# Performance work log

Measured on AMD Instinct MI355X. Metric: run time of the kernel, lower is better.

The kernel has to match this reference:

```python
import jax, jax.numpy as jnp
import numpy as np

EPS = 1e-5

def _ln(x):
    # F.layer_norm over last dim, no affine params
    m = jnp.mean(x, axis=-1, keepdims=True)
    v = jnp.mean((x - m) ** 2, axis=-1, keepdims=True)
    return (x - m) * jax.lax.rsqrt(v + EPS)

def _jagged_to_padded(vals, offsets, B, n):
    # vals: [T, F] -> [B, n, F], zero padded
    T = vals.shape[0]
    lengths = offsets[1:] - offsets[:-1]            # [B]
    pos = jnp.arange(n)
    idx = offsets[:-1, None] + pos[None, :]         # [B, n]
    valid = pos[None, :] < lengths[:, None]         # [B, n]
    gathered = vals[jnp.clip(idx, 0, T - 1)]        # [B, n, F]
    return jnp.where(valid[..., None], gathered, 0.0)

def _dense_to_jagged(padded, offsets, T):
    # padded: [B, n, F] -> [T, F]
    t = jnp.arange(T)
    b = jnp.clip(jnp.searchsorted(offsets, t, side='right') - 1, 0, offsets.shape[0] - 2)
    pos = t - offsets[b]
    return padded[b, pos]

def setup_inputs() -> dict:
    key = jax.random.key(0)
    D, H, d = 1024, 8, 128
    B, n = 4, 2048
    T = B * n  # all sequences full length
    ks = jax.random.split(key, 4)
    x = jax.random.normal(ks[0], (T, D), dtype=jnp.float32)
    attnmask = jnp.tril(jnp.ones((n, n), dtype=jnp.float32))
    x_offsets = jnp.arange(B + 1, dtype=jnp.int32) * n
    proj_w = jax.random.normal(ks[1], (D, H * d * 4), dtype=jnp.float32) * 0.02
    out_w = jax.random.normal(ks[2], (H * d, D), dtype=jnp.float32) * 0.02
    out_b = jnp.zeros((D,), dtype=jnp.float32)
    return {"x": x, "attnmask": attnmask, "proj_w": proj_w, "out_w": out_w,
            "out_b": out_b, "x_offsets": x_offsets, "B": B, "n": n}

def reference(x, attnmask, proj_w, out_w, out_b, x_offsets, B, n):
    T, D = x.shape
    H, d4 = 8, proj_w.shape[1] // 8
    d = d4 // 4
    x = _ln(x)
    h = jax.nn.silu(x @ proj_w).reshape(T, H, 4 * d)   # silu BEFORE split (HSTU)
    u, v, q, k = jnp.split(h, 4, axis=-1)              # each [T, H, d]
    pq = _jagged_to_padded(q.reshape(T, H * d), x_offsets, B, n).reshape(B, n, H, d)
    pk = _jagged_to_padded(k.reshape(T, H * d), x_offsets, B, n).reshape(B, n, H, d)
    pv = _jagged_to_padded(v.reshape(T, H * d), x_offsets, B, n).reshape(B, n, H, d)
    scores = jnp.einsum('bnhd,bmhd->bhnm', pq, pk)
    scores = jax.nn.silu(scores) / n * attnmask[None, None]
    attnout = jnp.einsum('bhnm,bmhd->bnhd', scores, pv).reshape(B, n, H * d)
    attnout = _dense_to_jagged(attnout, x_offsets, T)  # [T, H*d]
    attnout = _ln(attnout) * u.reshape(T, H * d)       # fused norm + gate
    return attnout @ out_w + out_b                      # out_proj (dropout inactive: eval)
```

## Files before the change

kernel.cpp:

```cpp
#include <hip/hip_runtime.h>

typedef short  s16x8 __attribute__((ext_vector_type(8)));
typedef float  f32x4 __attribute__((ext_vector_type(4)));
typedef unsigned short u16;
typedef unsigned int   u32;

#define T_TOK 8192
#define D_IN  1024
#define D4    4096
#define NH    8
#define DH    128
#define NSEQ  2048

__device__ __forceinline__ float u16f(u16 s){
  union { unsigned int u; float f; } c; c.u = ((unsigned int)s) << 16; return c.f;
}
__device__ __forceinline__ u16 f2u16(float f){
  union { float f; unsigned int u; } c; c.f = f;
  unsigned int r = (c.u + 0x7fffu + ((c.u >> 16) & 1u)) >> 16;
  return (u16)r;
}
__device__ __forceinline__ unsigned int cvt2_bf16(float a, float b){
  unsigned int r;
  asm("v_cvt_pk_bf16_f32 %0, %1, %2" : "=v"(r) : "v"(a), "v"(b));
  return r;
}
__device__ __forceinline__ float fast_silu(float v){
  return v * __builtin_amdgcn_rcpf(1.0f + __expf(-v));
}
__device__ __forceinline__ void gload_lds16(const u16* g, u16* lds){
  __builtin_amdgcn_global_load_lds(
      (const __attribute__((address_space(1))) u32*)g,
      (__attribute__((address_space(3))) u32*)lds, 16, 0, 0);
}

__device__ __forceinline__ void block_reduce2(float& a, float& b){
  __shared__ float red[8];
  #pragma unroll
  for (int off = 32; off > 0; off >>= 1){
    a += __shfl_down(a, off, 64);
    b += __shfl_down(b, off, 64);
  }
  int w = threadIdx.x >> 6;
  if ((threadIdx.x & 63) == 0){ red[w*2] = a; red[w*2+1] = b; }
  __syncthreads();
  a = red[0] + red[2] + red[4] + red[6];
  b = red[1] + red[3] + red[5] + red[7];
  __syncthreads();
}

__global__ void ln_x_kernel(const float* __restrict__ x, u16* __restrict__ xn){
  int t = blockIdx.x;
  const float* row = x + (size_t)t * D_IN;
  int base = threadIdx.x * 4;
  float4 v = *(const float4*)(row + base);
  float s = v.x + v.y + v.z + v.w;
  float q = v.x*v.x + v.y*v.y + v.z*v.z + v.w*v.w;
  block_reduce2(s, q);
  float mean = s * (1.0f / D_IN);
  float var  = q * (1.0f / D_IN) - mean * mean;
  float rstd = rsqrtf(var + 1e-5f);
  ushort4 o;
  o.x = f2u16((v.x - mean) * rstd); o.y = f2u16((v.y - mean) * rstd);
  o.z = f2u16((v.z - mean) * rstd); o.w = f2u16((v.w - mean) * rstd);
  *(ushort4*)(xn + (size_t)t * D_IN + base) = o;
}

__global__ void transpose_kernel(const float* __restrict__ in, u16* __restrict__ out,
                                 int R, int C){
  __shared__ u16 tile[32][33];
  int c0 = blockIdx.x * 32, r0 = blockIdx.y * 32;
  for (int i = threadIdx.y; i < 32; i += 8)
    tile[i][threadIdx.x] = f2u16(in[(size_t)(r0 + i) * C + c0 + threadIdx.x]);
  __syncthreads();
  for (int i = threadIdx.y; i < 32; i += 8)
    out[(size_t)(c0 + i) * R + r0 + threadIdx.x] = tile[threadIdx.x][i];
}

__global__ void vt_kernel(const u16* __restrict__ h, u16* __restrict__ vt){
  __shared__ u16 tile[32][33];
  int bh = blockIdx.z; int b = bh >> 3, hh = bh & 7;
  int p0 = blockIdx.x * 32, d0 = blockIdx.y * 32;
  const u16* src = h + (size_t)(b * NSEQ) * D4 + hh * 512 + 128;
  for (int i = threadIdx.y; i < 32; i += 8)
    tile[i][threadIdx.x] = src[(size_t)(p0 + i) * D4 + d0 + threadIdx.x];
  __syncthreads();
  u16* dst = vt + (size_t)bh * DH * NSEQ;
  for (int i = threadIdx.y; i < 32; i += 8)
    dst[(size_t)(d0 + i) * NSEQ + p0 + threadIdx.x] = tile[threadIdx.x][i];
}

template<int EPI>
__global__ __launch_bounds__(256, 2) void gemm_bt_kernel(
    const u16* __restrict__ A, const u16* __restrict__ Bt,
    const float* __restrict__ bias, u16* __restrict__ Cb, float* __restrict__ Cf,
    int M, int N, int K)
{
  __shared__ __align__(16) u16 As[128 * 64];
  __shared__ __align__(16) u16 Bs[128 * 64];
  int bn = blockIdx.x, bm = blockIdx.y;
  int tid = threadIdx.x;
  int lane = tid & 63, wave = tid >> 6;
  int lr = lane & 15, quad = lane >> 4;
  int wm = (wave >> 1) * 64, wn = (wave & 1) * 64;
  f32x4 acc[4][4] = {};

  int srow = lane >> 3;
  int scol = ((lane & 7) ^ srow) * 8;
  const u16* Ab = A  + (size_t)(bm * 128) * K;
  const u16* Bb = Bt + (size_t)(bn * 128) * K;
  int swz = (lr & 7) * 8;

  for (int k0 = 0; k0 < K; k0 += 64){
    #pragma unroll
    for (int it = 0; it < 4; ++it){
      int c = it * 4 + wave;
      gload_lds16(Ab + (size_t)(c * 8 + srow) * K + k0 + scol, As + c * 512);
    }
    #pragma unroll
    for (int it = 0; it < 4; ++it){
      int c = it * 4 + wave;
      gload_lds16(Bb + (size_t)(c * 8 + srow) * K + k0 + scol, Bs + c * 512);
    }
    __syncthreads();
    #pragma unroll
    for (int ks = 0; ks < 2; ++ks){
      s16x8 af[4], bf[4];
      #pragma unroll
      for (int i = 0; i < 4; ++i)
        af[i] = *(const s16x8*)&As[(wm + i*16 + lr) * 64 + (((ks*32 + quad*8)) ^ swz)];
      #pragma unroll
      for (int j = 0; j < 4; ++j)
        bf[j] = *(const s16x8*)&Bs[(wn + j*16 + lr) * 64 + (((ks*32 + quad*8)) ^ swz)];
      #pragma unroll
      for (int i = 0; i < 4; ++i)
        #pragma unroll
        for (int j = 0; j < 4; ++j)
          acc[i][j] = __builtin_amdgcn_mfma_f32_16x16x32_bf16(af[i], bf[j], acc[i][j], 0, 0, 0);
    }
    __syncthreads();
  }
  #pragma unroll
  for (int j = 0; j < 4; ++j){
    int nc = bn * 128 + wn + j * 16 + lr;
    float bv = 0.0f;
    if (EPI == 1) bv = bias[nc];
    #pragma unroll
    for (int i = 0; i < 4; ++i){
      #pragma unroll
      for (int r = 0; r < 4; ++r){
        int mr = bm * 128 + wm + i * 16 + quad * 4 + r;
        float v = acc[i][j][r];
        if (EPI == 0){
          v = fast_silu(v);
          Cb[(size_t)mr * N + nc] = f2u16(v);
        } else {
          Cf[(size_t)mr * N + nc] = v + bv;
        }
      }
    }
  }
}

__global__ __launch_bounds__(256, 2) void attn_kernel(
    const u16* __restrict__ h, const u16* __restrict__ vt, u16* __restrict__ ao)
{
  constexpr int KS_BYTES = 64 * 136 * 2;
  constexpr int VS_BYTES = 128 * 72 * 2;
  __shared__ __align__(16) char smem[KS_BYTES + 2 * VS_BYTES];
  u16 (*Ks)[136] = (u16(*)[136])smem;
  u16 (*Vs)[72]  = (u16(*)[72])(smem + KS_BYTES);
  u16 (*Ss)[72]  = (u16(*)[72])(smem + KS_BYTES + VS_BYTES);
  u16 (*Qs)[136] = (u16(*)[136])smem;

  int id = blockIdx.x;
  int qt, bh;
  if (id < 256) { qt = id & 15;        bh = id >> 4;          }
  else          { qt = 15 - (id & 15); bh = 16 + ((id - 256) >> 4); }
  int b = bh >> 3, hh = bh & 7;
  int tid = threadIdx.x;
  int lane = tid & 63, wave = tid >> 6;
  int lr = lane & 15, quad = lane >> 4;
  int wq = wave * 32;

  const u16* kbase = h  + (size_t)(b * NSEQ) * D4 + hh * 512 + 384;
  const u16* vbase = vt + (size_t)bh * DH * NSEQ;

  int krow = tid >> 4;
  int kcol = (tid & 15) * 8;
  int vrow = tid >> 3;
  int vcol = (tid & 7) * 8;

  const u16* qsrc = h + (size_t)(b * NSEQ + qt * 128) * D4 + hh * 512 + 256;
  #pragma unroll
  for (int it = 0; it < 8; ++it){
    int row = it * 16 + (tid >> 4), col = (tid & 15) * 8;
    *(uint4*)&Qs[row][col] = *(const uint4*)(qsrc + (size_t)row * D4 + col);
  }
  __syncthreads();
  s16x8 qf[2][4];
  #pragma unroll
  for (int i = 0; i < 2; ++i)
    #pragma unroll
    for (int ks = 0; ks < 4; ++ks)
      qf[i][ks] = *(const s16x8*)&Qs[wq + i*16 + lr][ks*32 + quad*8];
  __syncthreads();

  f32x4 oacc[2][8] = {};
  int nkt = 2 * qt + 2;

  for (int kt = 0; kt < nkt; ++kt){
    int k0 = kt * 64;
    #pragma unroll
    for (int it = 0; it < 4; ++it)
      *(uint4*)&Ks[it*16 + krow][kcol] =
          *(const uint4*)(kbase + (size_t)(k0 + it*16 + krow) * D4 + kcol);
    #pragma unroll
    for (int it = 0; it < 4; ++it)
      *(uint4*)&Vs[it*32 + vrow][vcol] =
          *(const uint4*)(vbase + (size_t)(it*32 + vrow) * NSEQ + k0 + vcol);
    __syncthreads();

    int lk0 = k0 - qt * 128;
    bool active = (lk0 < wq + 32);
    if (active){
      f32x4 sacc[2][4] = {};
      __builtin_amdgcn_s_setprio(1);
      #pragma unroll
      for (int ks = 0; ks < 4; ++ks){
        s16x8 kf[4];
        #pragma unroll
        for (int jb = 0; jb < 4; ++jb) kf[jb] = *(const s16x8*)&Ks[jb*16 + lr][ks*32 + quad*8];
        #pragma unroll
        for (int i = 0; i < 2; ++i)
          #pragma unroll
          for (int jb = 0; jb < 4; ++jb)
            sacc[i][jb] = __builtin_amdgcn_mfma_f32_16x16x32_bf16(qf[i][ks], kf[jb], sacc[i][jb], 0, 0, 0);
      }
      __builtin_amdgcn_s_setprio(0);

      bool needmask = (lk0 + 63 > wq);
      if (needmask){
        #pragma unroll
        for (int i = 0; i < 2; ++i)
          #pragma unroll
          for (int jb = 0; jb < 4; ++jb){
            int qbase = wq + i*16 + quad*4;
            float p[4];
            #pragma unroll
            for (int r = 0; r < 4; ++r){
              float v = fast_silu(sacc[i][jb][r]);
              if (lk0 + jb*16 + lr > qbase + r) v = 0.0f;
              p[r] = v;
            }
            unsigned int c01 = cvt2_bf16(p[0], p[1]);
            unsigned int c23 = cvt2_bf16(p[2], p[3]);
            Ss[qbase+0][jb*16+lr] = (u16)(c01);
            Ss[qbase+1][jb*16+lr] = (u16)(c01 >> 16);
            Ss[qbase+2][jb*16+lr] = (u16)(c23);
            Ss[qbase+3][jb*16+lr] = (u16)(c23 >> 16);
          }
      } else {
        #pragma unroll
        for (int i = 0; i < 2; ++i)
          #pragma unroll
          for (int jb = 0; jb < 4; ++jb){
            int qbase = wq + i*16 + quad*4;
            float p[4];
            #pragma unroll
            for (int r = 0; r < 4; ++r)
              p[r] = fast_silu(sacc[i][jb][r]);
            unsigned int c01 = cvt2_bf16(p[0], p[1]);
            unsigned int c23 = cvt2_bf16(p[2], p[3]);
            Ss[qbase+0][jb*16+lr] = (u16)(c01);
            Ss[qbase+1][jb*16+lr] = (u16)(c01 >> 16);
            Ss[qbase+2][jb*16+lr] = (u16)(c23);
            Ss[qbase+3][jb*16+lr] = (u16)(c23 >> 16);
          }
      }

      __builtin_amdgcn_s_setprio(1);
      #pragma unroll
      for (int ks = 0; ks < 2; ++ks){
        s16x8 pf[2], vf2[8];
        #pragma unroll
        for (int i = 0; i < 2; ++i) pf[i] = *(const s16x8*)&Ss[wq + i*16 + lr][ks*32 + quad*8];
        #pragma unroll
        for (int j = 0; j < 8; ++j) vf2[j] = *(const s16x8*)&Vs[j*16 + lr][ks*32 + quad*8];
        #pragma unroll
        for (int i = 0; i < 2; ++i)
          #pragma unroll
          for (int j = 0; j < 8; ++j)
            oacc[i][j] = __builtin_amdgcn_mfma_f32_16x16x32_bf16(pf[i], vf2[j], oacc[i][j], 0, 0, 0);
      }
      __builtin_amdgcn_s_setprio(0);
    }
    __syncthreads();
  }

  u16* aobase = ao + (size_t)(b * NSEQ + qt * 128) * D_IN + hh * DH;
  #pragma unroll
  for (int i = 0; i < 2; ++i)
    #pragma unroll
    for (int j = 0; j < 8; ++j){
      float s0 = oacc[i][j][0] * (1.0f / (float)NSEQ);
      float s1 = oacc[i][j][1] * (1.0f / (float)NSEQ);
      float s2 = oacc[i][j][2] * (1.0f / (float)NSEQ);
      float s3 = oacc[i][j][3] * (1.0f / (float)NSEQ);
      unsigned int c01 = cvt2_bf16(s0, s1);
      unsigned int c23 = cvt2_bf16(s2, s3);
      int rbase = wq + i*16 + quad*4;
      aobase[(size_t)(rbase+0) * D_IN + j*16 + lr] = (u16)(c01);
      aobase[(size_t)(rbase+1) * D_IN + j*16 + lr] = (u16)(c01 >> 16);
      aobase[(size_t)(rbase+2) * D_IN + j*16 + lr] = (u16)(c23);
      aobase[(size_t)(rbase+3) * D_IN + j*16 + lr] = (u16)(c23 >> 16);
    }
}

__global__ void ln_gate_kernel(const u16* __restrict__ ao, const u16* __restrict__ h,
                               u16* __restrict__ gated){
  int t = blockIdx.x;
  const u16* row = ao + (size_t)t * D_IN;
  int base = threadIdx.x * 4;
  ushort4 raw = *(const ushort4*)(row + base);
  float vx = u16f(raw.x), vy = u16f(raw.y), vz = u16f(raw.z), vw = u16f(raw.w);
  float s = vx + vy + vz + vw;
  float q = vx*vx + vy*vy + vz*vz + vw*vw;
  block_reduce2(s, q);
  float mean = s * (1.0f / D_IN);
  float var  = q * (1.0f / D_IN) - mean * mean;
  float rstd = rsqrtf(var + 1e-5f);
  ushort4 uu = *(const ushort4*)(h + (size_t)t * D4 + (base >> 7) * 512 + (base & 127));
  ushort4 o;
  o.x = f2u16((vx - mean) * rstd * u16f(uu.x));
  o.y = f2u16((vy - mean) * rstd * u16f(uu.y));
  o.z = f2u16((vz - mean) * rstd * u16f(uu.z));
  o.w = f2u16((vw - mean) * rstd * u16f(uu.w));
  *(ushort4*)(gated + (size_t)t * D_IN + base) = o;
}

extern "C" void kernel_launch(void* const* d_in, const int* in_sizes, int n_in,
                              void* d_out, int out_size, void* d_ws, size_t ws_size,
                              hipStream_t stream)
{
  (void)in_sizes; (void)n_in; (void)out_size; (void)ws_size;
  const float* x      = (const float*)d_in[0];
  const float* proj_w = (const float*)d_in[2];
  const float* out_w  = (const float*)d_in[3];
  const float* out_b  = (const float*)d_in[4];
  float* out = (float*)d_out;

  const size_t MB = 1024 * 1024;
  char* ws = (char*)d_ws;
  u16* xn  = (u16*)(ws);
  u16* h   = (u16*)(ws + 16 * MB);
  u16* Wt  = (u16*)(ws + 80 * MB);
  u16* OWt = (u16*)(ws + 88 * MB);
  u16* Vt  = (u16*)(ws + 90 * MB);
  u16* ao    = xn;
  u16* gated = Vt;

  dim3 tb32(32, 8);
  hipLaunchKernelGGL(transpose_kernel, dim3(D4 / 32, D_IN / 32), tb32, 0, stream,
                     proj_w, Wt, D_IN, D4);
  hipLaunchKernelGGL(transpose_kernel, dim3(D_IN / 32, D_IN / 32), tb32, 0, stream,
                     out_w, OWt, D_IN, D_IN);
  hipLaunchKernelGGL(ln_x_kernel, dim3(T_TOK), dim3(256), 0, stream, x, xn);
  hipLaunchKernelGGL(HIP_KERNEL_NAME(gemm_bt_kernel<0>), dim3(D4 / 128, T_TOK / 128),
                     dim3(256), 0, stream, xn, Wt, (const float*)nullptr, h,
                     (float*)nullptr, T_TOK, D4, D_IN);
  hipLaunchKernelGGL(vt_kernel, dim3(NSEQ / 32, DH / 32, 32), tb32, 0, stream, h, Vt);
  hipLaunchKernelGGL(attn_kernel, dim3(512), dim3(256), 0, stream, h, Vt, ao);
  hipLaunchKernelGGL(ln_gate_kernel, dim3(T_TOK), dim3(256), 0, stream, ao, h, gated);
  hipLaunchKernelGGL(HIP_KERNEL_NAME(gemm_bt_kernel<1>), dim3(D_IN / 128, T_TOK / 128),
                     dim3(256), 0, stream, gated, OWt, out_b, (u16*)nullptr,
                     out, T_TOK, D_IN, D_IN);
}
```

Baseline: 311.1 us.

## Double-buffer K/V tiles via direct global-to-LDS loads with XOR swizzle

Replaces the synchronous register-staged K/V tile loads in the attention kernel with asynchronous global-to-LDS loads into double buffers, prefetching the next tile while the current one is computed. The K, V and score tiles drop their padding and use XOR-swizzled layouts to avoid LDS bank conflicts. Q fragments are read straight from global memory into registers, skipping the LDS staging. LDS use grows to 80 KB per block, which may limit occupancy relative to the two-block launch bound, and correctness depends on the wait/barrier placement around the async loads.

```diff
diff --git a/kernel.cpp b/kernel.cpp
--- a/kernel.cpp
+++ b/kernel.cpp
@@ -165,13 +165,7 @@
 __global__ __launch_bounds__(256, 2) void attn_kernel(
     const u16* __restrict__ h, const u16* __restrict__ vt, u16* __restrict__ ao)
 {
-  constexpr int KS_BYTES = 64 * 136 * 2;
-  constexpr int VS_BYTES = 128 * 72 * 2;
-  __shared__ __align__(16) char smem[KS_BYTES + 2 * VS_BYTES];
-  u16 (*Ks)[136] = (u16(*)[136])smem;
-  u16 (*Vs)[72]  = (u16(*)[72])(smem + KS_BYTES);
-  u16 (*Ss)[72]  = (u16(*)[72])(smem + KS_BYTES + VS_BYTES);
-  u16 (*Qs)[136] = (u16(*)[136])smem;
+  __shared__ __align__(16) u16 smem[40960];
 
   int id = blockIdx.x;
   int qt, bh;
@@ -185,41 +179,48 @@
 
   const u16* kbase = h  + (size_t)(b * NSEQ) * D4 + hh * 512 + 384;
   const u16* vbase = vt + (size_t)bh * DH * NSEQ;
-
-  int krow = tid >> 4;
-  int kcol = (tid & 15) * 8;
-  int vrow = tid >> 3;
-  int vcol = (tid & 7) * 8;
+  u16* Ssl = smem + 32768;
+
+  auto stage = [&](int bufsel, int k0n){
+    u16* kd = smem + bufsel * 8192;
+    u16* vd = smem + 16384 + bufsel * 8192;
+    #pragma unroll
+    for (int it = 0; it < 4; ++it){
+      int c = it * 4 + wave;
+      int row = c * 4 + (lane >> 4);
+      int ss = (lane & 15) ^ (row & 15);
+      gload_lds16(kbase + (size_t)(k0n + row) * D4 + ss * 8, kd + c * 512);
+    }
+    #pragma unroll
+    for (int it = 0; it < 4; ++it){
+      int c = it * 4 + wave;
+      int row = c * 8 + (lane >> 3);
+      int ss = (lane & 7) ^ (lane >> 3);
+      gload_lds16(vbase + (size_t)row * NSEQ + k0n + ss * 8, vd + c * 512);
+    }
+  };
 
   const u16* qsrc = h + (size_t)(b * NSEQ + qt * 128) * D4 + hh * 512 + 256;
-  #pragma unroll
-  for (int it = 0; it < 8; ++it){
-    int row = it * 16 + (tid >> 4), col = (tid & 15) * 8;
-    *(uint4*)&Qs[row][col] = *(const uint4*)(qsrc + (size_t)row * D4 + col);
-  }
-  __syncthreads();
   s16x8 qf[2][4];
   #pragma unroll
   for (int i = 0; i < 2; ++i)
     #pragma unroll
     for (int ks = 0; ks < 4; ++ks)
-      qf[i][ks] = *(const s16x8*)&Qs[wq + i*16 + lr][ks*32 + quad*8];
+      qf[i][ks] = *(const s16x8*)(qsrc + (size_t)(wq + i*16 + lr) * D4 + ks*32 + quad*8);
+
+  stage(0, 0);
   __syncthreads();
 
   f32x4 oacc[2][8] = {};
   int nkt = 2 * qt + 2;
 
   for (int kt = 0; kt < nkt; ++kt){
+    int cur = kt & 1;
     int k0 = kt * 64;
-    #pragma unroll
-    for (int it = 0; it < 4; ++it)
-      *(uint4*)&Ks[it*16 + krow][kcol] =
-          *(const uint4*)(kbase + (size_t)(k0 + it*16 + krow) * D4 + kcol);
-    #pragma unroll
-    for (int it = 0; it < 4; ++it)
-      *(uint4*)&Vs[it*32 + vrow][vcol] =
-          *(const uint4*)(vbase + (size_t)(it*32 + vrow) * NSEQ + k0 + vcol);
-    __syncthreads();
+    if (kt + 1 < nkt) stage(cur ^ 1, k0 + 64);
+
+    const u16* kc = smem + cur * 8192;
+    const u16* vc = smem + 16384 + cur * 8192;
 
     int lk0 = k0 - qt * 128;
     bool active = (lk0 < wq + 32);
@@ -230,7 +231,8 @@
       for (int ks = 0; ks < 4; ++ks){
         s16x8 kf[4];
         #pragma unroll
-        for (int jb = 0; jb < 4; ++jb) kf[jb] = *(const s16x8*)&Ks[jb*16 + lr][ks*32 + quad*8];
+        for (int jb = 0; jb < 4; ++jb)
+          kf[jb] = *(const s16x8*)&kc[(jb*16 + lr) * 128 + (((ks*4 + quad) ^ lr) << 3)];
         #pragma unroll
         for (int i = 0; i < 2; ++i)
           #pragma unroll
@@ -240,53 +242,44 @@
       __builtin_amdgcn_s_setprio(0);
 
       bool needmask = (lk0 + 63 > wq);
-      if (needmask){
-        #pragma unroll
-        for (int i = 0; i < 2; ++i)
-          #pragma unroll
-          for (int jb = 0; jb < 4; ++jb){
-            int qbase = wq + i*16 + quad*4;
-            float p[4];
+      #pragma unroll
+      for (int i = 0; i < 2; ++i)
+        #pragma unroll
+        for (int jb = 0; jb < 4; ++jb){
+          int qbase = wq + i*16 + quad*4;
+          int slot = jb*2 + (lr >> 3);
+          int off  = lr & 7;
+          float p[4];
+          if (needmask){
             #pragma unroll
             for (int r = 0; r < 4; ++r){
               float v = fast_silu(sacc[i][jb][r]);
               if (lk0 + jb*16 + lr > qbase + r) v = 0.0f;
               p[r] = v;
             }
-            unsigned int c01 = cvt2_bf16(p[0], p[1]);
-            unsigned int c23 = cvt2_bf16(p[2], p[3]);
-            Ss[qbase+0][jb*16+lr] = (u16)(c01);
-            Ss[qbase+1][jb*16+lr] = (u16)(c01 >> 16);
-            Ss[qbase+2][jb*16+lr] = (u16)(c23);
-            Ss[qbase+3][jb*16+lr] = (u16)(c23 >> 16);
-          }
-      } else {
-        #pragma unroll
-        for (int i = 0; i < 2; ++i)
-          #pragma unroll
-          for (int jb = 0; jb < 4; ++jb){
-            int qbase = wq + i*16 + quad*4;
-            float p[4];
+          } else {
             #pragma unroll
             for (int r = 0; r < 4; ++r)
               p[r] = fast_silu(sacc[i][jb][r]);
-            unsigned int c01 = cvt2_bf16(p[0], p[1]);
-            unsigned int c23 = cvt2_bf16(p[2], p[3]);
-            Ss[qbase+0][jb*16+lr] = (u16)(c01);
-            Ss[qbase+1][jb*16+lr] = (u16)(c01 >> 16);
-            Ss[qbase+2][jb*16+lr] = (u16)(c23);
-            Ss[qbase+3][jb*16+lr] = (u16)(c23 >> 16);
           }
-      }
+          unsigned int c01 = cvt2_bf16(p[0], p[1]);
+          unsigned int c23 = cvt2_bf16(p[2], p[3]);
+          Ssl[(qbase+0)*64 + (((slot ^ ((qbase+0)&7)) << 3) | off)] = (u16)(c01);
+          Ssl[(qbase+1)*64 + (((slot ^ ((qbase+1)&7)) << 3) | off)] = (u16)(c01 >> 16);
+          Ssl[(qbase+2)*64 + (((slot ^ ((qbase+2)&7)) << 3) | off)] = (u16)(c23);
+          Ssl[(qbase+3)*64 + (((slot ^ ((qbase+3)&7)) << 3) | off)] = (u16)(c23 >> 16);
+        }
 
       __builtin_amdgcn_s_setprio(1);
       #pragma unroll
       for (int ks = 0; ks < 2; ++ks){
         s16x8 pf[2], vf2[8];
         #pragma unroll
-        for (int i = 0; i < 2; ++i) pf[i] = *(const s16x8*)&Ss[wq + i*16 + lr][ks*32 + quad*8];
-        #pragma unroll
-        for (int j = 0; j < 8; ++j) vf2[j] = *(const s16x8*)&Vs[j*16 + lr][ks*32 + quad*8];
+        for (int i = 0; i < 2; ++i)
+          pf[i] = *(const s16x8*)&Ssl[(wq + i*16 + lr) * 64 + (((ks*4 + quad) ^ (lr & 7)) << 3)];
+        #pragma unroll
+        for (int j = 0; j < 8; ++j)
+          vf2[j] = *(const s16x8*)&vc[(j*16 + lr) * 64 + (((ks*4 + quad) ^ (lr & 7)) << 3)];
         #pragma unroll
         for (int i = 0; i < 2; ++i)
           #pragma unroll
```

Result: slower. 319.4 us (+2.7%).
